# Performance work log

Measured on AMD Instinct MI355X. Metric: run time of the kernel, lower is better.

Reference implementation:

```python
import jax, jax.numpy as jnp
import numpy as np

N = 100_000          # nodes
E = 1_600_000        # edges (avg degree 16)
IN_C, OUT_C = 256, 128


def setup_inputs() -> dict:
    key = jax.random.key(0)
    k1, k2, k3, k4, k5 = jax.random.split(key, 5)
    X = jax.random.normal(k1, (N, IN_C), dtype=jnp.float32)
    # nn.Linear(in, out, bias=False) weight has shape [out, in]
    W = jax.random.normal(k2, (OUT_C, IN_C), dtype=jnp.float32) * (1.0 / np.sqrt(IN_C))
    A_rows = jnp.sort(jax.random.randint(k3, (E,), 0, N, dtype=jnp.int32))
    A_cols = jax.random.randint(k4, (E,), 0, N, dtype=jnp.int32)
    # positive values mimicking symmetric-normalized adjacency entries
    A_vals = jax.random.uniform(k5, (E,), dtype=jnp.float32) * (1.0 / 16.0)
    return {"X": X, "W": W, "A_rows": A_rows, "A_cols": A_cols, "A_vals": A_vals}


def reference(X, W, A_rows, A_cols, A_vals):
    # X = self._linear(X)  ->  X @ W^T   [N, OUT_C]
    H = jnp.einsum("ni,oi->no", X, W)
    # X = torch.sparse.mm(A_hat, X): out[r] += v * H[c] for each edge (r, c, v)
    msgs = A_vals[:, None] * H[A_cols]                      # [E, OUT_C]
    out = jax.ops.segment_sum(msgs, A_rows, num_segments=N)  # [N, OUT_C]
    return out
```

## Files before the change

### kernel.cpp

```cpp
#include <hip/hip_runtime.h>
#include <hip/hip_bf16.h>

#define NNODES 100000
#define NEDGES 1600000
#define IN_C   256
#define OUT_C  128

typedef short bf16x8 __attribute__((ext_vector_type(8)));
typedef float f32x4  __attribute__((ext_vector_type(4)));

static __device__ __forceinline__ unsigned short f2bf(float f) {
    union { float f; unsigned u; } c; c.f = f;
    unsigned r = c.u + 0x7fffu + ((c.u >> 16) & 1u);
    return (unsigned short)(r >> 16);
}
static __device__ __forceinline__ float bflo(unsigned u) {
    union { unsigned u; float f; } c; c.u = u << 16; return c.f;
}
static __device__ __forceinline__ float bfhi(unsigned u) {
    union { unsigned u; float f; } c; c.u = u & 0xffff0000u; return c.f;
}

__global__ __launch_bounds__(256) void gemm_xwt(const float* __restrict__ X,
                                                const float* __restrict__ W,
                                                unsigned short* __restrict__ H) {
    __shared__ unsigned short Xs[128 * 128];
    __shared__ unsigned short Wsh[128 * 128];

    const int tid  = threadIdx.x;
    const int lane = tid & 63;
    const int wid  = tid >> 6;
    const int wr   = (wid >> 1) * 64;
    const int wc   = (wid & 1) * 64;
    const int row0 = blockIdx.x * 128;

    f32x4 acc[4][4] = {};

    for (int kc = 0; kc < IN_C; kc += 128) {
#pragma unroll
        for (int p = 0; p < 16; ++p) {
            int idx = p * 256 + tid;
            int r   = idx >> 5;
            int c4  = idx & 31;
            float4 v = make_float4(0.f, 0.f, 0.f, 0.f);
            int grow = row0 + r;
            if (grow < NNODES)
                v = *(const float4*)(X + (size_t)grow * IN_C + kc + c4 * 4);
            int byte = (r * 256 + c4 * 8) ^ ((r & 7) << 4);
            *(ushort4*)((char*)Xs + byte) =
                make_ushort4(f2bf(v.x), f2bf(v.y), f2bf(v.z), f2bf(v.w));
        }
#pragma unroll
        for (int p = 0; p < 16; ++p) {
            int idx = p * 256 + tid;
            int o   = idx >> 5;
            int c4  = idx & 31;
            float4 v = *(const float4*)(W + (size_t)o * IN_C + kc + c4 * 4);
            int byte = (o * 256 + c4 * 8) ^ ((o & 7) << 4);
            *(ushort4*)((char*)Wsh + byte) =
                make_ushort4(f2bf(v.x), f2bf(v.y), f2bf(v.z), f2bf(v.w));
        }
        __syncthreads();

#pragma unroll
        for (int ks = 0; ks < 4; ++ks) {
            const int kb = ks * 64 + (lane >> 4) * 16;
            bf16x8 a[4], b[4];
#pragma unroll
            for (int m = 0; m < 4; ++m) {
                int r    = wr + m * 16 + (lane & 15);
                int byte = (r * 256 + kb) ^ ((r & 7) << 4);
                a[m] = *(const bf16x8*)((const char*)Xs + byte);
            }
#pragma unroll
            for (int n = 0; n < 4; ++n) {
                int o    = wc + n * 16 + (lane & 15);
                int byte = (o * 256 + kb) ^ ((o & 7) << 4);
                b[n] = *(const bf16x8*)((const char*)Wsh + byte);
            }
#pragma unroll
            for (int m = 0; m < 4; ++m)
#pragma unroll
                for (int n = 0; n < 4; ++n)
                    acc[m][n] = __builtin_amdgcn_mfma_f32_16x16x32_bf16(
                        a[m], b[n], acc[m][n], 0, 0, 0);
        }
        __syncthreads();
    }

#pragma unroll
    for (int m = 0; m < 4; ++m) {
#pragma unroll
        for (int r = 0; r < 4; ++r) {
            int grow = row0 + wr + m * 16 + (lane >> 4) * 4 + r;
            if (grow < NNODES) {
#pragma unroll
                for (int n = 0; n < 4; ++n) {
                    int col = wc + n * 16 + (lane & 15);
                    H[(size_t)grow * OUT_C + col] = f2bf(acc[m][n][r]);
                }
            }
        }
    }
}

__global__ __launch_bounds__(256) void build_rowptr(const int* __restrict__ rows,
                                                    int* __restrict__ rowptr) {
    int r = blockIdx.x * 256 + threadIdx.x;
    if (r > NNODES) return;
    int lo = 0, hi = NEDGES;
    while (lo < hi) {
        int mid = (lo + hi) >> 1;
        if (rows[mid] < r) lo = mid + 1; else hi = mid;
    }
    rowptr[r] = lo;
}

__global__ __launch_bounds__(256) void spmm_rows(const uint4* __restrict__ H4,
                                                 const int* __restrict__ rowptr,
                                                 const int* __restrict__ cols,
                                                 const float* __restrict__ vals,
                                                 float* __restrict__ out) {
    const int wid  = threadIdx.x >> 6;
    const int lane = threadIdx.x & 63;
    const int row  = blockIdx.x * 4 + wid;
    if (row >= NNODES) return;

    const int s  = rowptr[row];
    const int e  = rowptr[row + 1];
    const int g  = lane >> 4;
    const int cg = lane & 15;

    float acc[8];
#pragma unroll
    for (int t = 0; t < 8; ++t) acc[t] = 0.f;

    for (int base = s; base < e; base += 64) {
        const int cnt = (e - base < 64) ? (e - base) : 64;
        int   ec = 0;
        float ev = 0.f;
        if (lane < cnt) { ec = cols[base + lane]; ev = vals[base + lane]; }

        int j = 0;
        for (; j + 16 <= cnt; j += 16) {
#pragma unroll
            for (int q = 0; q < 4; ++q) {
                int   c = __shfl(ec, j + q * 4 + g);
                float v = __shfl(ev, j + q * 4 + g);
                uint4 u = H4[(size_t)c * 16 + cg];
                acc[0] += v * bflo(u.x); acc[1] += v * bfhi(u.x);
                acc[2] += v * bflo(u.y); acc[3] += v * bfhi(u.y);
                acc[4] += v * bflo(u.z); acc[5] += v * bfhi(u.z);
                acc[6] += v * bflo(u.w); acc[7] += v * bfhi(u.w);
            }
        }
        for (; j < cnt; j += 4) {
            int   c = __shfl(ec, j + g);
            float v = __shfl(ev, j + g);
            uint4 u = H4[(size_t)c * 16 + cg];
            acc[0] += v * bflo(u.x); acc[1] += v * bfhi(u.x);
            acc[2] += v * bflo(u.y); acc[3] += v * bfhi(u.y);
            acc[4] += v * bflo(u.z); acc[5] += v * bfhi(u.z);
            acc[6] += v * bflo(u.w); acc[7] += v * bfhi(u.w);
        }
    }

#pragma unroll
    for (int t = 0; t < 8; ++t) {
        acc[t] += __shfl_xor(acc[t], 16);
        acc[t] += __shfl_xor(acc[t], 32);
    }
    if (lane < 16) {
        float4 v0 = make_float4(acc[0], acc[1], acc[2], acc[3]);
        float4 v1 = make_float4(acc[4], acc[5], acc[6], acc[7]);
        *(float4*)(out + (size_t)row * OUT_C + cg * 8)     = v0;
        *(float4*)(out + (size_t)row * OUT_C + cg * 8 + 4) = v1;
    }
}

extern "C" void kernel_launch(void* const* d_in, const int* in_sizes, int n_in,
                              void* d_out, int out_size, void* d_ws, size_t ws_size,
                              hipStream_t stream) {
    const float* X      = (const float*)d_in[0];
    const float* W      = (const float*)d_in[1];
    const int*   A_rows = (const int*)d_in[2];
    const int*   A_cols = (const int*)d_in[3];
    const float* A_vals = (const float*)d_in[4];
    float* out = (float*)d_out;

    unsigned short* H   = (unsigned short*)d_ws;
    int* rowptr = (int*)((char*)d_ws +
                         (size_t)NNODES * OUT_C * sizeof(unsigned short));

    gemm_xwt<<<(NNODES + 127) / 128, 256, 0, stream>>>(X, W, H);
    build_rowptr<<<(NNODES + 1 + 255) / 256, 256, 0, stream>>>(A_rows, rowptr);
    spmm_rows<<<(NNODES + 3) / 4, 256, 0, stream>>>((const uint4*)H, rowptr,
                                                    A_cols, A_vals, out);
}
```

Before: 107.8 us.

## Keep W fragments in registers and tile GEMM as 64 rows by full K

The GEMM kernel now uses 512-thread blocks over 64-row tiles. Each of the 8 waves loads and converts its own 16 output columns of W straight into registers, so W no longer goes through shared memory. X is staged once for the full K=256 in a single shared buffer, which removes the K-loop and its extra barriers, and the smaller LDS footprint allows more blocks per CU. The cost is that every block re-reads and re-converts W from global/L2, each wave runs fewer MFMAs, and the H stores become scattered 2-byte writes.

```diff
diff --git a/kernel.cpp b/kernel.cpp
--- a/kernel.cpp
+++ b/kernel.cpp
@@ -21,85 +21,67 @@
     union { unsigned u; float f; } c; c.u = u & 0xffff0000u; return c.f;
 }
 
-__global__ __launch_bounds__(256) void gemm_xwt(const float* __restrict__ X,
-                                                const float* __restrict__ W,
-                                                unsigned short* __restrict__ H) {
-    __shared__ unsigned short Xs[128 * 128];
-    __shared__ unsigned short Wsh[128 * 128];
+union BF8 { bf16x8 v; unsigned short s[8]; };
+
+__global__ __launch_bounds__(512, 4) void gemm_xwt(const float* __restrict__ X,
+                                                   const float* __restrict__ W,
+                                                   unsigned short* __restrict__ H) {
+    __shared__ unsigned short Xs[64 * 256];
 
     const int tid  = threadIdx.x;
     const int lane = tid & 63;
     const int wid  = tid >> 6;
-    const int wr   = (wid >> 1) * 64;
-    const int wc   = (wid & 1) * 64;
-    const int row0 = blockIdx.x * 128;
+    const int row0 = blockIdx.x * 64;
+    const int wr   = lane & 15;
+    const int ko   = (lane >> 4) * 8;
 
-    f32x4 acc[4][4] = {};
-
-    for (int kc = 0; kc < IN_C; kc += 128) {
+    bf16x8 wf[8];
 #pragma unroll
-        for (int p = 0; p < 16; ++p) {
-            int idx = p * 256 + tid;
-            int r   = idx >> 5;
-            int c4  = idx & 31;
-            float4 v = make_float4(0.f, 0.f, 0.f, 0.f);
-            int grow = row0 + r;
-            if (grow < NNODES)
-                v = *(const float4*)(X + (size_t)grow * IN_C + kc + c4 * 4);
-            int byte = (r * 256 + c4 * 8) ^ ((r & 7) << 4);
-            *(ushort4*)((char*)Xs + byte) =
-                make_ushort4(f2bf(v.x), f2bf(v.y), f2bf(v.z), f2bf(v.w));
-        }
-#pragma unroll
-        for (int p = 0; p < 16; ++p) {
-            int idx = p * 256 + tid;
-            int o   = idx >> 5;
-            int c4  = idx & 31;
-            float4 v = *(const float4*)(W + (size_t)o * IN_C + kc + c4 * 4);
-            int byte = (o * 256 + c4 * 8) ^ ((o & 7) << 4);
-            *(ushort4*)((char*)Wsh + byte) =
-                make_ushort4(f2bf(v.x), f2bf(v.y), f2bf(v.z), f2bf(v.w));
-        }
-        __syncthreads();
+    for (int ks = 0; ks < 8; ++ks) {
+        const float* src = W + (size_t)(wid * 16 + wr) * IN_C + ks * 32 + ko;
+        float4 a = *(const float4*)src;
+        float4 b = *(const float4*)(src + 4);
+        BF8 t;
+        t.s[0] = f2bf(a.x); t.s[1] = f2bf(a.y); t.s[2] = f2bf(a.z); t.s[3] = f2bf(a.w);
+        t.s[4] = f2bf(b.x); t.s[5] = f2bf(b.y); t.s[6] = f2bf(b.z); t.s[7] = f2bf(b.w);
+        wf[ks] = t.v;
+    }
 
 #pragma unroll
-        for (int ks = 0; ks < 4; ++ks) {
-            const int kb = ks * 64 + (lane >> 4) * 16;
-            bf16x8 a[4], b[4];
+    for (int p = 0; p < 8; ++p) {
+        int idx = p * 512 + tid;
+        int r   = idx >> 6;
+        int c4  = idx & 63;
+        float4 v = make_float4(0.f, 0.f, 0.f, 0.f);
+        if (row0 + r < NNODES)
+            v = *(const float4*)(X + (size_t)(row0 + r) * IN_C + c4 * 4);
+        int byte = (r * 512 + c4 * 8) ^ ((r & 7) << 4);
+        *(ushort4*)((char*)Xs + byte) =
+            make_ushort4(f2bf(v.x), f2bf(v.y), f2bf(v.z), f2bf(v.w));
+    }
+    __syncthreads();
+
+    f32x4 acc[4] = {};
 #pragma unroll
-            for (int m = 0; m < 4; ++m) {
-                int r    = wr + m * 16 + (lane & 15);
-                int byte = (r * 256 + kb) ^ ((r & 7) << 4);
-                a[m] = *(const bf16x8*)((const char*)Xs + byte);
-            }
+    for (int ks = 0; ks < 8; ++ks) {
+        const int kb = ks * 64 + (lane >> 4) * 16;
 #pragma unroll
-            for (int n = 0; n < 4; ++n) {
-                int o    = wc + n * 16 + (lane & 15);
-                int byte = (o * 256 + kb) ^ ((o & 7) << 4);
-                b[n] = *(const bf16x8*)((const char*)Wsh + byte);
-            }
-#pragma unroll
-            for (int m = 0; m < 4; ++m)
-#pragma unroll
-                for (int n = 0; n < 4; ++n)
-                    acc[m][n] = __builtin_amdgcn_mfma_f32_16x16x32_bf16(
-                        a[m], b[n], acc[m][n], 0, 0, 0);
+        for (int m = 0; m < 4; ++m) {
+            int r    = m * 16 + wr;
+            int byte = (r * 512 + kb) ^ ((r & 7) << 4);
+            bf16x8 a = *(const bf16x8*)((const char*)Xs + byte);
+            acc[m] = __builtin_amdgcn_mfma_f32_16x16x32_bf16(a, wf[ks], acc[m],
+                                                             0, 0, 0);
         }
-        __syncthreads();
     }
 
 #pragma unroll
     for (int m = 0; m < 4; ++m) {
 #pragma unroll
         for (int r = 0; r < 4; ++r) {
-            int grow = row0 + wr + m * 16 + (lane >> 4) * 4 + r;
-            if (grow < NNODES) {
-#pragma unroll
-                for (int n = 0; n < 4; ++n) {
-                    int col = wc + n * 16 + (lane & 15);
-                    H[(size_t)grow * OUT_C + col] = f2bf(acc[m][n][r]);
-                }
-            }
+            int grow = row0 + m * 16 + (lane >> 4) * 4 + r;
+            if (grow < NNODES)
+                H[(size_t)grow * OUT_C + wid * 16 + wr] = f2bf(acc[m][r]);
         }
     }
 }
@@ -192,7 +174,7 @@
     int* rowptr = (int*)((char*)d_ws +
                          (size_t)NNODES * OUT_C * sizeof(unsigned short));
 
-    gemm_xwt<<<(NNODES + 127) / 128, 256, 0, stream>>>(X, W, H);
+    gemm_xwt<<<(NNODES + 63) / 64, 512, 0, stream>>>(X, W, H);
     build_rowptr<<<(NNODES + 1 + 255) / 256, 256, 0, stream>>>(A_rows, rowptr);
     spmm_rows<<<(NNODES + 3) / 4, 256, 0, stream>>>((const uint4*)H, rowptr,
                                                     A_cols, A_vals, out);
```

New measurement: 117.3 us. 8.8% more time.
